# Kernel tuning notes

Measured on AMD Instinct MI355X. Metric: run time of the kernel, lower is better.

## Reference

```python
import jax, jax.numpy as jnp
import numpy as np


def _graph_conv(feat_src, e_src, e_dst, n_src, n_dst, W, b):
    # DGL GraphConv, norm='both', bipartite block; feat_src: [N_src, A, C, H]
    ones_e = jnp.ones(e_src.shape[0], dtype=feat_src.dtype)
    out_deg = jax.ops.segment_sum(ones_e, e_src, num_segments=n_src)
    in_deg = jax.ops.segment_sum(ones_e, e_dst, num_segments=n_dst)
    norm_src = jnp.clip(out_deg, 1.0) ** -0.5
    norm_dst = jnp.clip(in_deg, 1.0) ** -0.5
    feat = feat_src * norm_src[:, None, None, None]
    # in_feats == out_feats -> DGL multiplies by W before aggregation
    feat = jnp.einsum('nach,ho->naco', feat, W)
    msgs = feat[e_src]                                   # gather  [E, A, C, H]
    agg = jax.ops.segment_sum(msgs, e_dst, num_segments=n_dst)  # scatter-add
    return agg * norm_dst[:, None, None, None] + b


def setup_inputs() -> dict:
    key = jax.random.key(0)
    ks = jax.random.split(key, 8)
    H = 128
    N_SRC0, N_DST0, N_DST1 = 50000, 20000, 4096
    E0, E1 = 320000, 65536
    return {
        'in_feat': jax.random.normal(ks[0], (2, H, 2, N_SRC0), dtype=jnp.float32),
        'W': jax.random.normal(ks[1], (H, H), dtype=jnp.float32) / np.sqrt(H),
        'b': jnp.zeros((H,), dtype=jnp.float32),
        'e0_src': jax.random.randint(ks[2], (E0,), 0, N_SRC0, dtype=jnp.int32),
        'e0_dst': jax.random.randint(ks[3], (E0,), 0, N_DST0, dtype=jnp.int32),
        'e1_src': jax.random.randint(ks[4], (E1,), 0, N_DST0, dtype=jnp.int32),
        'e1_dst': jax.random.randint(ks[5], (E1,), 0, N_DST1, dtype=jnp.int32),
        'n_dst0': N_DST0,
        'n_dst1': N_DST1,
    }


def reference(in_feat, W, b, e0_src, e0_dst, e1_src, e1_dst, n_dst0, n_dst1):
    # [A, H, C, N] -> [N, A, C, H]
    x = jnp.transpose(in_feat, (3, 0, 2, 1))
    n_src0 = x.shape[0]
    h = _graph_conv(x, e0_src, e0_dst, n_src0, n_dst0, W, b)
    h = jax.nn.relu(h)
    h = _graph_conv(h, e1_src, e1_dst, n_dst0, n_dst1, W, b)
    h = jax.nn.relu(h)
    # [N_dst1, A, C, H] -> [A, H, C, N_dst1]
    out = jnp.transpose(h, (1, 3, 2, 0))
    return jax.nn.relu(out)
```

## Files before the change

### kernel.cpp

```cpp
#include <hip/hip_runtime.h>
#include <math.h>

#define H128 128
#define NF 512
typedef unsigned short u16;

__device__ inline u16 f2bf(float f) {
  union { float f; unsigned u; } x; x.f = f;
  unsigned r = x.u + 0x7FFFu + ((x.u >> 16) & 1u);
  return (u16)(r >> 16);
}
__device__ inline void addbf8(float* a, uint4 u) {
  a[0] += __uint_as_float(u.x << 16);
  a[1] += __uint_as_float(u.x & 0xFFFF0000u);
  a[2] += __uint_as_float(u.y << 16);
  a[3] += __uint_as_float(u.y & 0xFFFF0000u);
  a[4] += __uint_as_float(u.z << 16);
  a[5] += __uint_as_float(u.z & 0xFFFF0000u);
  a[6] += __uint_as_float(u.w << 16);
  a[7] += __uint_as_float(u.w & 0xFFFF0000u);
}

__global__ void k_count4(const int* __restrict__ e0s, const int* __restrict__ e0d,
                         const int* __restrict__ e1s, const int* __restrict__ e1d,
                         int E0, int E1,
                         int* __restrict__ c_s0, int* __restrict__ c_d0,
                         int* __restrict__ c_s1, int* __restrict__ c_d1) {
  int i = blockIdx.x * 256 + threadIdx.x;
  if (i < E0) { atomicAdd(&c_s0[e0s[i]], 1); return; }
  i -= E0;
  if (i < E0) { atomicAdd(&c_d0[e0d[i]], 1); return; }
  i -= E0;
  if (i < E1) { atomicAdd(&c_s1[e1s[i]], 1); return; }
  i -= E1;
  if (i < E1) { atomicAdd(&c_d1[e1d[i]], 1); }
}

__global__ void k_norm(int* __restrict__ buf, int n) {
  int i = blockIdx.x * 256 + threadIdx.x;
  if (i < n) {
    int d = buf[i];
    float dv = (d < 1) ? 1.0f : (float)d;
    ((float*)buf)[i] = 1.0f / sqrtf(dv);
  }
}

__global__ void k_scan(const int* __restrict__ degA, int nA, int* __restrict__ offA, int* __restrict__ curA,
                       const int* __restrict__ degB, int nB, int* __restrict__ offB, int* __restrict__ curB) {
  const int* deg = blockIdx.x ? degB : degA;
  int n = blockIdx.x ? nB : nA;
  int* off = blockIdx.x ? offB : offA;
  int* cur = blockIdx.x ? curB : curA;
  __shared__ int wsum[16];
  __shared__ int s_carry;
  const int tid = threadIdx.x;
  const int lane = tid & 63;
  const int wv = tid >> 6;
  if (tid == 0) s_carry = 0;
  __syncthreads();
  for (int base = 0; base < n; base += 1024) {
    int i = base + tid;
    int v = (i < n) ? deg[i] : 0;
    int x = v;
    #pragma unroll
    for (int d2 = 1; d2 < 64; d2 <<= 1) {
      int y = __shfl_up(x, (unsigned)d2, 64);
      if (lane >= d2) x += y;
    }
    if (lane == 63) wsum[wv] = x;
    __syncthreads();
    if (wv == 0 && lane < 16) {
      int w = wsum[lane];
      #pragma unroll
      for (int d2 = 1; d2 < 16; d2 <<= 1) {
        int y = __shfl_up(w, (unsigned)d2, 64);
        if (lane >= d2) w += y;
      }
      wsum[lane] = w;
    }
    __syncthreads();
    int waveoff = (wv == 0) ? 0 : wsum[wv - 1];
    int excl = s_carry + waveoff + x - v;
    if (i < n) { off[i] = excl; cur[i] = excl; }
    __syncthreads();
    if (tid == 0) s_carry += wsum[15];
    __syncthreads();
  }
  if (tid == 0) off[n] = s_carry;
}

__global__ void k_scatter2(const int* __restrict__ e0s, const int* __restrict__ e0d,
                           const int* __restrict__ e1s, const int* __restrict__ e1d,
                           int E0, int E1,
                           int* __restrict__ cur0, int* __restrict__ csr0,
                           int* __restrict__ cur1, int* __restrict__ csr1) {
  int i = blockIdx.x * 256 + threadIdx.x;
  if (i < E0) {
    int p = atomicAdd(&cur0[e0d[i]], 1);
    csr0[p] = e0s[i];
    return;
  }
  i -= E0;
  if (i < E1) {
    int p = atomicAdd(&cur1[e1d[i]], 1);
    csr1[p] = e1s[i];
  }
}

__global__ __launch_bounds__(256) void k_transpose_in(
    const float* __restrict__ in, const float* __restrict__ norm,
    u16* __restrict__ xp, int N) {
  __shared__ float tile[64][132];
  const int tid = threadIdx.x;
  const int n0 = blockIdx.x << 6;
  const int ac = blockIdx.y;
  const int a = ac >> 1, c = ac & 1;
  const float* base = in + ((size_t)a * 256 + c) * (size_t)N;
  #pragma unroll
  for (int i = 0; i < 8; ++i) {
    int fidx = (i << 8) + tid;
    int h = fidx >> 4;
    int n = (fidx & 15) << 2;
    int gn = n0 + n;
    float4 v = make_float4(0.f, 0.f, 0.f, 0.f);
    if (gn < N) v = *(const float4*)(base + (size_t)h * 2 * N + gn);
    tile[n + 0][h] = v.x; tile[n + 1][h] = v.y;
    tile[n + 2][h] = v.z; tile[n + 3][h] = v.w;
  }
  __syncthreads();
  #pragma unroll
  for (int i = 0; i < 8; ++i) {
    int fidx = (i << 8) + tid;
    int h4 = fidx & 31;
    int n = fidx >> 5;
    int gn = n0 + n;
    if (gn < N) {
      float4 v = *(const float4*)(&tile[n][h4 << 2]);
      float s = norm[gn];
      ushort4 o;
      o.x = f2bf(v.x * s); o.y = f2bf(v.y * s);
      o.z = f2bf(v.z * s); o.w = f2bf(v.w * s);
      *(ushort4*)(xp + (size_t)gn * NF + ac * H128 + (h4 << 2)) = o;
    }
  }
}

__global__ __launch_bounds__(256) void k_agg(
    const u16* __restrict__ xp, const int* __restrict__ csr,
    const int* __restrict__ off, const float* __restrict__ norm_dst,
    float* __restrict__ outp, int ndst) {
  const int wave = threadIdx.x >> 6;
  const int lane = threadIdx.x & 63;
  const int d = blockIdx.x * 4 + wave;
  if (d >= ndst) return;
  const int s = off[d], e = off[d + 1];
  float acc[8];
  #pragma unroll
  for (int i = 0; i < 8; ++i) acc[i] = 0.f;
  int j = s;
  for (; j + 4 <= e; j += 4) {
    int s0 = csr[j], s1 = csr[j + 1], s2 = csr[j + 2], s3 = csr[j + 3];
    uint4 u0 = *((const uint4*)(xp + (size_t)s0 * NF) + lane);
    uint4 u1 = *((const uint4*)(xp + (size_t)s1 * NF) + lane);
    uint4 u2 = *((const uint4*)(xp + (size_t)s2 * NF) + lane);
    uint4 u3 = *((const uint4*)(xp + (size_t)s3 * NF) + lane);
    addbf8(acc, u0); addbf8(acc, u1); addbf8(acc, u2); addbf8(acc, u3);
  }
  for (; j < e; ++j) {
    uint4 u = *((const uint4*)(xp + (size_t)csr[j] * NF) + lane);
    addbf8(acc, u);
  }
  float nd = norm_dst[d];
  float* orow = outp + (size_t)d * NF + lane * 8;
  float4 o0 = make_float4(acc[0] * nd, acc[1] * nd, acc[2] * nd, acc[3] * nd);
  float4 o1 = make_float4(acc[4] * nd, acc[5] * nd, acc[6] * nd, acc[7] * nd);
  *(float4*)orow = o0;
  *(float4*)(orow + 4) = o1;
}

template <int BR, int RT, bool OUT_BF16>
__global__ __launch_bounds__(256) void k_gemm(
    const float* __restrict__ A, const float* __restrict__ W,
    const float* __restrict__ bias, const float* __restrict__ scale,
    void* __restrict__ outv, int M) {
  __shared__ float As[32][BR + 4];
  __shared__ float Ws[32][132];
  const int tid = threadIdx.x;
  const int tx = tid & 15;
  const int ty = tid >> 4;
  const int c0 = tx << 2;
  const int row0 = blockIdx.x * BR;
  float acc[RT][8];
  #pragma unroll
  for (int r = 0; r < RT; ++r)
    #pragma unroll
    for (int c = 0; c < 8; ++c) acc[r][c] = 0.f;

  for (int kc = 0; kc < 128; kc += 32) {
    __syncthreads();
    #pragma unroll
    for (int i = 0; i < 4; ++i) {
      int fidx = (i << 8) + tid;
      int k = fidx >> 5, cq = fidx & 31;
      *(float4*)(&Ws[k][cq << 2]) = *(const float4*)(W + (size_t)(kc + k) * 128 + (cq << 2));
    }
    #pragma unroll
    for (int i = 0; i < BR / 32; ++i) {
      int fidx = (i << 8) + tid;
      int r = fidx >> 3, kq = fidx & 7;
      int row = row0 + r;
      float4 v = make_float4(0.f, 0.f, 0.f, 0.f);
      if (row < M) v = *(const float4*)(A + (size_t)row * 128 + kc + (kq << 2));
      int k = kq << 2;
      As[k + 0][r] = v.x; As[k + 1][r] = v.y;
      As[k + 2][r] = v.z; As[k + 3][r] = v.w;
    }
    __syncthreads();
    #pragma unroll 4
    for (int k = 0; k < 32; ++k) {
      float4 w0 = *(const float4*)(&Ws[k][c0]);
      float4 w1 = *(const float4*)(&Ws[k][64 + c0]);
      float a[RT];
      #pragma unroll
      for (int rr = 0; rr < RT / 4; ++rr) {
        float4 av = *(const float4*)(&As[k][ty * RT + (rr << 2)]);
        a[rr * 4 + 0] = av.x; a[rr * 4 + 1] = av.y;
        a[rr * 4 + 2] = av.z; a[rr * 4 + 3] = av.w;
      }
      #pragma unroll
      for (int r = 0; r < RT; ++r) {
        acc[r][0] = fmaf(a[r], w0.x, acc[r][0]);
        acc[r][1] = fmaf(a[r], w0.y, acc[r][1]);
        acc[r][2] = fmaf(a[r], w0.z, acc[r][2]);
        acc[r][3] = fmaf(a[r], w0.w, acc[r][3]);
        acc[r][4] = fmaf(a[r], w1.x, acc[r][4]);
        acc[r][5] = fmaf(a[r], w1.y, acc[r][5]);
        acc[r][6] = fmaf(a[r], w1.z, acc[r][6]);
        acc[r][7] = fmaf(a[r], w1.w, acc[r][7]);
      }
    }
  }
  float4 b0 = *(const float4*)(bias + c0);
  float4 b1 = *(const float4*)(bias + 64 + c0);
  #pragma unroll
  for (int r = 0; r < RT; ++r) {
    int row = row0 + ty * RT + r;
    if (row < M) {
      float sc = scale ? scale[row >> 2] : 1.f;
      float v[8];
      v[0] = acc[r][0] + b0.x; v[1] = acc[r][1] + b0.y;
      v[2] = acc[r][2] + b0.z; v[3] = acc[r][3] + b0.w;
      v[4] = acc[r][4] + b1.x; v[5] = acc[r][5] + b1.y;
      v[6] = acc[r][6] + b1.z; v[7] = acc[r][7] + b1.w;
      #pragma unroll
      for (int c = 0; c < 8; ++c) v[c] = (v[c] > 0.f ? v[c] : 0.f) * sc;
      if (OUT_BF16) {
        u16* out = (u16*)outv;
        ushort4 q0, q1;
        q0.x = f2bf(v[0]); q0.y = f2bf(v[1]); q0.z = f2bf(v[2]); q0.w = f2bf(v[3]);
        q1.x = f2bf(v[4]); q1.y = f2bf(v[5]); q1.z = f2bf(v[6]); q1.w = f2bf(v[7]);
        *(ushort4*)(out + (size_t)row * 128 + c0) = q0;
        *(ushort4*)(out + (size_t)row * 128 + 64 + c0) = q1;
      } else {
        float* out = (float*)outv;
        *(float4*)(out + (size_t)row * 128 + c0) = make_float4(v[0], v[1], v[2], v[3]);
        *(float4*)(out + (size_t)row * 128 + 64 + c0) = make_float4(v[4], v[5], v[6], v[7]);
      }
    }
  }
}

__global__ __launch_bounds__(256) void k_transpose_out(
    const float* __restrict__ h1, float* __restrict__ out, int N) {
  __shared__ float tile[128][68];
  const int tid = threadIdx.x;
  const int n0 = blockIdx.x << 6;
  const int ac = blockIdx.y;
  const int a = ac >> 1, c = ac & 1;
  #pragma unroll
  for (int i = 0; i < 8; ++i) {
    int fidx = (i << 8) + tid;
    int h4 = fidx & 31;
    int n = fidx >> 5;
    float4 v = *(const float4*)(h1 + (size_t)(n0 + n) * NF + ac * H128 + (h4 << 2));
    int h = h4 << 2;
    tile[h + 0][n] = v.x; tile[h + 1][n] = v.y;
    tile[h + 2][n] = v.z; tile[h + 3][n] = v.w;
  }
  __syncthreads();
  float* obase = out + ((size_t)a * 256 + c) * (size_t)N;
  #pragma unroll
  for (int i = 0; i < 8; ++i) {
    int fidx = (i << 8) + tid;
    int h = fidx >> 4;
    int n = (fidx & 15) << 2;
    float4 v = *(const float4*)(&tile[h][n]);
    *(float4*)(obase + (size_t)h * 2 * N + n0 + n) = v;
  }
}

extern "C" void kernel_launch(void* const* d_in, const int* in_sizes, int n_in,
                              void* d_out, int out_size, void* d_ws, size_t ws_size,
                              hipStream_t stream) {
  const float* in_feat = (const float*)d_in[0];
  const float* W       = (const float*)d_in[1];
  const float* bias    = (const float*)d_in[2];
  const int* e0_src    = (const int*)d_in[3];
  const int* e0_dst    = (const int*)d_in[4];
  const int* e1_src    = (const int*)d_in[5];
  const int* e1_dst    = (const int*)d_in[6];
  const int N_DST0 = 20000;
  const int N_DST1 = 4096;
  const int N_SRC0 = in_sizes[0] / NF;
  const int E0 = in_sizes[3];
  const int E1 = in_sizes[5];

  u16* xp    = (u16*)d_ws;
  float* agg0 = (float*)(xp + (size_t)N_SRC0 * NF);
  u16* h0    = xp;
  float* agg1 = (float*)(xp + (size_t)N_DST0 * NF);
  float* h1   = agg1 + (size_t)N_DST1 * NF;
  int* ibase    = (int*)(agg0 + (size_t)N_DST0 * NF);
  int* cnt_src0 = ibase;
  int* cnt_dst0 = cnt_src0 + N_SRC0;
  int* cnt_src1 = cnt_dst0 + N_DST0;
  int* cnt_dst1 = cnt_src1 + N_DST0;
  int* off0 = cnt_dst1 + N_DST1;
  int* cur0 = off0 + N_DST0 + 1;
  int* csr0 = cur0 + N_DST0;
  int* off1 = csr0 + E0;
  int* cur1 = off1 + N_DST1 + 1;
  int* csr1 = cur1 + N_DST1;

  const int NCNT = N_SRC0 + N_DST0 + N_DST0 + N_DST1;
  hipMemsetAsync(cnt_src0, 0, (size_t)NCNT * sizeof(int), stream);

  int tot_cnt = 2 * E0 + 2 * E1;
  k_count4<<<(tot_cnt + 255) / 256, 256, 0, stream>>>(
      e0_src, e0_dst, e1_src, e1_dst, E0, E1, cnt_src0, cnt_dst0, cnt_src1, cnt_dst1);

  k_scan<<<2, 1024, 0, stream>>>(cnt_dst0, N_DST0, off0, cur0,
                                 cnt_dst1, N_DST1, off1, cur1);

  k_norm<<<(NCNT + 255) / 256, 256, 0, stream>>>(cnt_src0, NCNT);

  k_scatter2<<<(E0 + E1 + 255) / 256, 256, 0, stream>>>(
      e0_src, e0_dst, e1_src, e1_dst, E0, E1, cur0, csr0, cur1, csr1);

  dim3 tg1((N_SRC0 + 63) / 64, 4);
  k_transpose_in<<<tg1, 256, 0, stream>>>(in_feat, (const float*)cnt_src0, xp, N_SRC0);

  k_agg<<<(N_DST0 + 3) / 4, 256, 0, stream>>>(xp, csr0, off0, (const float*)cnt_dst0, agg0, N_DST0);

  k_gemm<128, 8, true><<<(N_DST0 * 4) / 128, 256, 0, stream>>>(
      agg0, W, bias, (const float*)cnt_src1, (void*)h0, N_DST0 * 4);

  k_agg<<<(N_DST1 + 3) / 4, 256, 0, stream>>>(h0, csr1, off1, (const float*)cnt_dst1, agg1, N_DST1);

  k_gemm<64, 4, false><<<(N_DST1 * 4) / 64, 256, 0, stream>>>(
      agg1, W, bias, nullptr, (void*)h1, N_DST1 * 4);

  dim3 tg2(N_DST1 / 64, 4);
  k_transpose_out<<<tg2, 256, 0, stream>>>(h1, (float*)d_out, N_DST1);
}
```

Before: 385.2 us.

## Fuse neighbor aggregation with the weight GEMM into one kernel

Merges the gather/sum aggregation kernel and the following 128x128 GEMM into one kernel per layer. Each block aggregates 16 destination nodes (64 rows) straight into shared memory and multiplies them by W there. This drops the fp32 agg intermediate round trip through global memory and two kernel launches per layer. In exchange each block holds a large shared tile (about 50KB), which may lower occupancy during the latency-bound gather phase, and the grid is much smaller for layer 1.

```diff
diff --git a/kernel.cpp b/kernel.cpp
--- a/kernel.cpp
+++ b/kernel.cpp
@@ -145,56 +145,58 @@
   }
 }
 
-__global__ __launch_bounds__(256) void k_agg(
+template <bool OUT_BF16>
+__global__ __launch_bounds__(256) void k_aggemm(
     const u16* __restrict__ xp, const int* __restrict__ csr,
     const int* __restrict__ off, const float* __restrict__ norm_dst,
-    float* __restrict__ outp, int ndst) {
-  const int wave = threadIdx.x >> 6;
-  const int lane = threadIdx.x & 63;
-  const int d = blockIdx.x * 4 + wave;
-  if (d >= ndst) return;
-  const int s = off[d], e = off[d + 1];
-  float acc[8];
-  #pragma unroll
-  for (int i = 0; i < 8; ++i) acc[i] = 0.f;
-  int j = s;
-  for (; j + 4 <= e; j += 4) {
-    int s0 = csr[j], s1 = csr[j + 1], s2 = csr[j + 2], s3 = csr[j + 3];
-    uint4 u0 = *((const uint4*)(xp + (size_t)s0 * NF) + lane);
-    uint4 u1 = *((const uint4*)(xp + (size_t)s1 * NF) + lane);
-    uint4 u2 = *((const uint4*)(xp + (size_t)s2 * NF) + lane);
-    uint4 u3 = *((const uint4*)(xp + (size_t)s3 * NF) + lane);
-    addbf8(acc, u0); addbf8(acc, u1); addbf8(acc, u2); addbf8(acc, u3);
-  }
-  for (; j < e; ++j) {
-    uint4 u = *((const uint4*)(xp + (size_t)csr[j] * NF) + lane);
-    addbf8(acc, u);
-  }
-  float nd = norm_dst[d];
-  float* orow = outp + (size_t)d * NF + lane * 8;
-  float4 o0 = make_float4(acc[0] * nd, acc[1] * nd, acc[2] * nd, acc[3] * nd);
-  float4 o1 = make_float4(acc[4] * nd, acc[5] * nd, acc[6] * nd, acc[7] * nd);
-  *(float4*)orow = o0;
-  *(float4*)(orow + 4) = o1;
-}
-
-template <int BR, int RT, bool OUT_BF16>
-__global__ __launch_bounds__(256) void k_gemm(
-    const float* __restrict__ A, const float* __restrict__ W,
-    const float* __restrict__ bias, const float* __restrict__ scale,
-    void* __restrict__ outv, int M) {
-  __shared__ float As[32][BR + 4];
+    const float* __restrict__ Wg, const float* __restrict__ bias,
+    const float* __restrict__ scale, void* __restrict__ outv, int ndst) {
+  __shared__ float As[64][132];
   __shared__ float Ws[32][132];
   const int tid = threadIdx.x;
+  const int wave = tid >> 6;
+  const int lane = tid & 63;
+  const int d0 = blockIdx.x * 16;
+
+  #pragma unroll
+  for (int i = 0; i < 4; ++i) {
+    int dl = wave + (i << 2);
+    int d = d0 + dl;
+    float acc[8];
+    #pragma unroll
+    for (int q = 0; q < 8; ++q) acc[q] = 0.f;
+    float nd = 0.f;
+    if (d < ndst) {
+      int s = off[d], e = off[d + 1];
+      nd = norm_dst[d];
+      int j = s;
+      for (; j + 4 <= e; j += 4) {
+        int s0 = csr[j], s1 = csr[j + 1], s2 = csr[j + 2], s3 = csr[j + 3];
+        uint4 u0 = *((const uint4*)(xp + (size_t)s0 * NF) + lane);
+        uint4 u1 = *((const uint4*)(xp + (size_t)s1 * NF) + lane);
+        uint4 u2 = *((const uint4*)(xp + (size_t)s2 * NF) + lane);
+        uint4 u3 = *((const uint4*)(xp + (size_t)s3 * NF) + lane);
+        addbf8(acc, u0); addbf8(acc, u1); addbf8(acc, u2); addbf8(acc, u3);
+      }
+      for (; j < e; ++j) {
+        uint4 u = *((const uint4*)(xp + (size_t)csr[j] * NF) + lane);
+        addbf8(acc, u);
+      }
+    }
+    int row_l = (dl << 2) + (lane >> 4);
+    int k0 = (lane & 15) << 3;
+    *(float4*)(&As[row_l][k0]) = make_float4(acc[0] * nd, acc[1] * nd, acc[2] * nd, acc[3] * nd);
+    *(float4*)(&As[row_l][k0 + 4]) = make_float4(acc[4] * nd, acc[5] * nd, acc[6] * nd, acc[7] * nd);
+  }
+
   const int tx = tid & 15;
   const int ty = tid >> 4;
   const int c0 = tx << 2;
-  const int row0 = blockIdx.x * BR;
-  float acc[RT][8];
-  #pragma unroll
-  for (int r = 0; r < RT; ++r)
-    #pragma unroll
-    for (int c = 0; c < 8; ++c) acc[r][c] = 0.f;
+  float gacc[4][8];
+  #pragma unroll
+  for (int r = 0; r < 4; ++r)
+    #pragma unroll
+    for (int c = 0; c < 8; ++c) gacc[r][c] = 0.f;
 
   for (int kc = 0; kc < 128; kc += 32) {
     __syncthreads();
@@ -202,56 +204,49 @@
     for (int i = 0; i < 4; ++i) {
       int fidx = (i << 8) + tid;
       int k = fidx >> 5, cq = fidx & 31;
-      *(float4*)(&Ws[k][cq << 2]) = *(const float4*)(W + (size_t)(kc + k) * 128 + (cq << 2));
-    }
-    #pragma unroll
-    for (int i = 0; i < BR / 32; ++i) {
-      int fidx = (i << 8) + tid;
-      int r = fidx >> 3, kq = fidx & 7;
-      int row = row0 + r;
-      float4 v = make_float4(0.f, 0.f, 0.f, 0.f);
-      if (row < M) v = *(const float4*)(A + (size_t)row * 128 + kc + (kq << 2));
-      int k = kq << 2;
-      As[k + 0][r] = v.x; As[k + 1][r] = v.y;
-      As[k + 2][r] = v.z; As[k + 3][r] = v.w;
-    }
-    __syncthreads();
-    #pragma unroll 4
-    for (int k = 0; k < 32; ++k) {
-      float4 w0 = *(const float4*)(&Ws[k][c0]);
-      float4 w1 = *(const float4*)(&Ws[k][64 + c0]);
-      float a[RT];
+      *(float4*)(&Ws[k][cq << 2]) = *(const float4*)(Wg + (size_t)(kc + k) * 128 + (cq << 2));
+    }
+    __syncthreads();
+    #pragma unroll
+    for (int k4 = 0; k4 < 32; k4 += 4) {
+      float4 av[4];
       #pragma unroll
-      for (int rr = 0; rr < RT / 4; ++rr) {
-        float4 av = *(const float4*)(&As[k][ty * RT + (rr << 2)]);
-        a[rr * 4 + 0] = av.x; a[rr * 4 + 1] = av.y;
-        a[rr * 4 + 2] = av.z; a[rr * 4 + 3] = av.w;
-      }
+      for (int rr = 0; rr < 4; ++rr)
+        av[rr] = *(const float4*)(&As[ty + (rr << 4)][kc + k4]);
       #pragma unroll
-      for (int r = 0; r < RT; ++r) {
-        acc[r][0] = fmaf(a[r], w0.x, acc[r][0]);
-        acc[r][1] = fmaf(a[r], w0.y, acc[r][1]);
-        acc[r][2] = fmaf(a[r], w0.z, acc[r][2]);
-        acc[r][3] = fmaf(a[r], w0.w, acc[r][3]);
-        acc[r][4] = fmaf(a[r], w1.x, acc[r][4]);
-        acc[r][5] = fmaf(a[r], w1.y, acc[r][5]);
-        acc[r][6] = fmaf(a[r], w1.z, acc[r][6]);
-        acc[r][7] = fmaf(a[r], w1.w, acc[r][7]);
-      }
-    }
-  }
+      for (int kk = 0; kk < 4; ++kk) {
+        float4 w0 = *(const float4*)(&Ws[k4 + kk][c0]);
+        float4 w1 = *(const float4*)(&Ws[k4 + kk][64 + c0]);
+        #pragma unroll
+        for (int rr = 0; rr < 4; ++rr) {
+          float a = (kk == 0) ? av[rr].x : (kk == 1) ? av[rr].y
+                  : (kk == 2) ? av[rr].z : av[rr].w;
+          gacc[rr][0] = fmaf(a, w0.x, gacc[rr][0]);
+          gacc[rr][1] = fmaf(a, w0.y, gacc[rr][1]);
+          gacc[rr][2] = fmaf(a, w0.z, gacc[rr][2]);
+          gacc[rr][3] = fmaf(a, w0.w, gacc[rr][3]);
+          gacc[rr][4] = fmaf(a, w1.x, gacc[rr][4]);
+          gacc[rr][5] = fmaf(a, w1.y, gacc[rr][5]);
+          gacc[rr][6] = fmaf(a, w1.z, gacc[rr][6]);
+          gacc[rr][7] = fmaf(a, w1.w, gacc[rr][7]);
+        }
+      }
+    }
+  }
+
   float4 b0 = *(const float4*)(bias + c0);
   float4 b1 = *(const float4*)(bias + 64 + c0);
-  #pragma unroll
-  for (int r = 0; r < RT; ++r) {
-    int row = row0 + ty * RT + r;
+  const int M = ndst << 2;
+  #pragma unroll
+  for (int rr = 0; rr < 4; ++rr) {
+    int row = (blockIdx.x << 6) + ty + (rr << 4);
     if (row < M) {
       float sc = scale ? scale[row >> 2] : 1.f;
       float v[8];
-      v[0] = acc[r][0] + b0.x; v[1] = acc[r][1] + b0.y;
-      v[2] = acc[r][2] + b0.z; v[3] = acc[r][3] + b0.w;
-      v[4] = acc[r][4] + b1.x; v[5] = acc[r][5] + b1.y;
-      v[6] = acc[r][6] + b1.z; v[7] = acc[r][7] + b1.w;
+      v[0] = gacc[rr][0] + b0.x; v[1] = gacc[rr][1] + b0.y;
+      v[2] = gacc[rr][2] + b0.z; v[3] = gacc[rr][3] + b0.w;
+      v[4] = gacc[rr][4] + b1.x; v[5] = gacc[rr][5] + b1.y;
+      v[6] = gacc[rr][6] + b1.z; v[7] = gacc[rr][7] + b1.w;
       #pragma unroll
       for (int c = 0; c < 8; ++c) v[c] = (v[c] > 0.f ? v[c] : 0.f) * sc;
       if (OUT_BF16) {
@@ -315,12 +310,10 @@
   const int E0 = in_sizes[3];
   const int E1 = in_sizes[5];
 
-  u16* xp    = (u16*)d_ws;
-  float* agg0 = (float*)(xp + (size_t)N_SRC0 * NF);
-  u16* h0    = xp;
-  float* agg1 = (float*)(xp + (size_t)N_DST0 * NF);
-  float* h1   = agg1 + (size_t)N_DST1 * NF;
-  int* ibase    = (int*)(agg0 + (size_t)N_DST0 * NF);
+  u16* xp = (u16*)d_ws;
+  u16* h0 = xp + (size_t)N_SRC0 * NF;
+  float* h1 = (float*)(h0 + (size_t)N_DST0 * NF);
+  int* ibase    = (int*)(h1 + (size_t)N_DST1 * NF);
   int* cnt_src0 = ibase;
   int* cnt_dst0 = cnt_src0 + N_SRC0;
   int* cnt_src1 = cnt_dst0 + N_DST0;
@@ -350,15 +343,13 @@
   dim3 tg1((N_SRC0 + 63) / 64, 4);
   k_transpose_in<<<tg1, 256, 0, stream>>>(in_feat, (const float*)cnt_src0, xp, N_SRC0);
 
-  k_agg<<<(N_DST0 + 3) / 4, 256, 0, stream>>>(xp, csr0, off0, (const float*)cnt_dst0, agg0, N_DST0);
-
-  k_gemm<128, 8, true><<<(N_DST0 * 4) / 128, 256, 0, stream>>>(
-      agg0, W, bias, (const float*)cnt_src1, (void*)h0, N_DST0 * 4);
-
-  k_agg<<<(N_DST1 + 3) / 4, 256, 0, stream>>>(h0, csr1, off1, (const float*)cnt_dst1, agg1, N_DST1);
-
-  k_gemm<64, 4, false><<<(N_DST1 * 4) / 64, 256, 0, stream>>>(
-      agg1, W, bias, nullptr, (void*)h1, N_DST1 * 4);
+  k_aggemm<true><<<N_DST0 / 16, 256, 0, stream>>>(
+      xp, csr0, off0, (const float*)cnt_dst0, W, bias,
+      (const float*)cnt_src1, (void*)h0, N_DST0);
+
+  k_aggemm<false><<<N_DST1 / 16, 256, 0, stream>>>(
+      h0, csr1, off1, (const float*)cnt_dst1, W, bias,
+      nullptr, (void*)h1, N_DST1);
 
   dim3 tg2(N_DST1 / 64, 4);
   k_transpose_out<<<tg2, 256, 0, stream>>>(h1, (float*)d_out, N_DST1);
```

After: 384.8 us. About the same (-0.1%).
